# Kernel optimization log

Hardware: AMD Instinct MI355X
Metric: run time of the kernel (lower is better)

## Reference

```python
import jax, jax.numpy as jnp
import numpy as np

N_NODES = 100000
DROP_P = 0.1


def gcn_conv(x, W, b, row, col, n_nodes):
    """PyG GCNConv: out = D^{-1/2}(A+I)D^{-1/2} X W + b.
    row/col already include self-loops. Messages flow row(src) -> col(dst)."""
    xw = x @ W  # [N, H]
    deg = jax.ops.segment_sum(jnp.ones_like(col, dtype=xw.dtype), col, num_segments=n_nodes)
    dinv = jnp.where(deg > 0, jax.lax.rsqrt(deg), 0.0)
    norm = dinv[row] * dinv[col]  # [E]
    msg = norm[:, None] * xw[row]  # [E, H] gather + scale
    out = jax.ops.segment_sum(msg, col, num_segments=n_nodes)  # scatter-add
    return out + b


def dropout(x, key, p):
    keep = jax.random.bernoulli(key, 1.0 - p, x.shape)
    return jnp.where(keep, x / (1.0 - p), 0.0).astype(x.dtype)


def prelu(x, alpha):
    return jnp.where(x >= 0, x, alpha[None, :] * x)


def setup_inputs() -> dict:
    key = jax.random.key(0)
    k1, k2, k3, k4 = jax.random.split(key, 4)
    in_ch, hid = 128, 128
    n_edges = 1600000
    x = jax.random.normal(k1, (N_NODES, in_ch), dtype=jnp.float32)
    edge_index = jax.random.randint(k2, (2, n_edges), 0, N_NODES, dtype=jnp.int64)
    s = 1.0 / np.sqrt(in_ch)
    W1 = jax.random.normal(k3, (in_ch, hid), dtype=jnp.float32) * s
    W2 = jax.random.normal(k4, (hid, hid), dtype=jnp.float32) * s
    b1 = jnp.zeros((hid,), dtype=jnp.float32)
    b2 = jnp.zeros((hid,), dtype=jnp.float32)
    alpha = jnp.full((hid,), 0.25, dtype=jnp.float32)
    return {"x": x, "edge_index": edge_index, "W1": W1, "b1": b1,
            "W2": W2, "b2": b2, "alpha": alpha}


def reference(x, edge_index, W1, b1, W2, b2, alpha):
    n = x.shape[0]
    # add self-loops once (PyG default add_self_loops=True)
    loop = jnp.arange(n, dtype=edge_index.dtype)
    row = jnp.concatenate([edge_index[0], loop])
    col = jnp.concatenate([edge_index[1], loop])

    dk1, dk2 = jax.random.split(jax.random.key(42))
    h = gcn_conv(x, W1, b1, row, col, n)
    h = dropout(h, dk1, DROP_P)
    h = prelu(h, alpha)
    h = gcn_conv(h, W2, b2, row, col, n)
    h = dropout(h, dk2, DROP_P)
    h = prelu(h, alpha)
    return h
```

## Files before the change

kernel.cpp:

```cpp
#include <hip/hip_runtime.h>
#include <stdint.h>
#include <string.h>

__host__ __device__ inline uint32_t rotl32(uint32_t x, int r) {
    return (x << r) | (x >> (32 - r));
}

__host__ __device__ inline void tf2x32(uint32_t k0, uint32_t k1,
                                       uint32_t x0, uint32_t x1,
                                       uint32_t& o0, uint32_t& o1) {
    uint32_t ks0 = k0, ks1 = k1, ks2 = k0 ^ k1 ^ 0x1BD11BDAu;
    x0 += ks0; x1 += ks1;
#define TF_R4(a,b,c,d) \
    x0 += x1; x1 = rotl32(x1,a); x1 ^= x0; \
    x0 += x1; x1 = rotl32(x1,b); x1 ^= x0; \
    x0 += x1; x1 = rotl32(x1,c); x1 ^= x0; \
    x0 += x1; x1 = rotl32(x1,d); x1 ^= x0;
    TF_R4(13,15,26,6)  x0 += ks1; x1 += ks2 + 1u;
    TF_R4(17,29,16,24) x0 += ks2; x1 += ks0 + 2u;
    TF_R4(13,15,26,6)  x0 += ks0; x1 += ks1 + 3u;
    TF_R4(17,29,16,24) x0 += ks1; x1 += ks2 + 4u;
    TF_R4(13,15,26,6)  x0 += ks2; x1 += ks0 + 5u;
#undef TF_R4
    o0 = x0; o1 = x1;
}

__device__ inline unsigned pk2h(float a, float b) {
    _Float16 ha = (_Float16)a, hb = (_Float16)b;
    unsigned short ua, ub;
    __builtin_memcpy(&ua, &ha, 2);
    __builtin_memcpy(&ub, &hb, 2);
    return (unsigned)ua | ((unsigned)ub << 16);
}
__device__ inline unsigned short h16bits(float a) {
    _Float16 h = (_Float16)a;
    unsigned short u; __builtin_memcpy(&u, &h, 2);
    return u;
}
__device__ inline float lo16(unsigned u) {
    unsigned short s = (unsigned short)(u & 0xffffu);
    _Float16 h; __builtin_memcpy(&h, &s, 2);
    return (float)h;
}
__device__ inline float hi16(unsigned u) {
    unsigned short s = (unsigned short)(u >> 16);
    _Float16 h; __builtin_memcpy(&h, &s, 2);
    return (float)h;
}

typedef float fx4 __attribute__((ext_vector_type(4)));
typedef unsigned ux4 __attribute__((ext_vector_type(4)));
typedef _Float16 h16x8 __attribute__((ext_vector_type(8)));
typedef _Float16 h16x2 __attribute__((ext_vector_type(2)));
typedef float f32x4 __attribute__((ext_vector_type(4)));

__device__ inline h16x2 as_h2(unsigned u) { h16x2 r; __builtin_memcpy(&r, &u, 4); return r; }

#define CSR_CAP 48
#define NSUP 8

__global__ __launch_bounds__(256) void k_build(
        const int* __restrict__ ei, int2* __restrict__ gsup,
        unsigned* __restrict__ gsupcnt,
        unsigned long long* __restrict__ m1, unsigned long long* __restrict__ m2,
        const float* __restrict__ x, unsigned* __restrict__ xb,
        const float* __restrict__ w1, const float* __restrict__ w2,
        _Float16* __restrict__ wt1, _Float16* __restrict__ wt2,
        unsigned k1a, unsigned k1b, unsigned k2a, unsigned k2b,
        int E, int N, int supw, int scap, int total,
        int P1A, int MB, int CB) {
    int b = blockIdx.x;
    int t = (int)threadIdx.x;
    if (b < P1A) {
        __shared__ unsigned hcnt[NSUP], hoff[NSUP], hrun[NSUP];
        if (t < NSUP) { hcnt[t] = 0; hrun[t] = 0; }
        __syncthreads();
        int e0 = b * 2048 + t;
        int r[8], c[8];
        unsigned sp[8];
#pragma unroll
        for (int i = 0; i < 8; i++) {
            int e = e0 + i * 256;
            sp[i] = 0xffu;
            if (e < E) {
                c[i] = __builtin_nontemporal_load(ei + (size_t)E + e);
                r[i] = __builtin_nontemporal_load(ei + e);
                if ((unsigned)c[i] < (unsigned)N && (unsigned)r[i] < (unsigned)N) {
                    sp[i] = (unsigned)c[i] / (unsigned)supw;
                    atomicAdd(&hcnt[sp[i]], 1u);
                }
            }
        }
        __syncthreads();
        if (t < NSUP) hoff[t] = atomicAdd(&gsupcnt[t], hcnt[t]);
        __syncthreads();
#pragma unroll
        for (int i = 0; i < 8; i++) {
            if (sp[i] < (unsigned)NSUP) {
                unsigned rank = atomicAdd(&hrun[sp[i]], 1u);
                unsigned gp = hoff[sp[i]] + rank;
                if (gp < (unsigned)scap)
                    gsup[(size_t)sp[i] * scap + gp] = make_int2(r[i], c[i]);
            }
        }
        return;
    }
    b -= P1A;
    if (b < MB) {
        int wv = (b * 256 + t) >> 6;
        int lane = t & 63;
        int TW = (2 * total) >> 6;
        int half = total >> 6;
        int w0 = wv * 8;
#pragma unroll
        for (int j = 0; j < 8; j++) {
            int wd = w0 + j;
            if (wd < TW) {
                int wl = wd;
                unsigned ka = k1a, kb = k1b;
                unsigned long long* m = m1;
                if (wl >= half) { wl -= half; ka = k2a; kb = k2b; m = m2; }
                uint32_t o0, o1;
                tf2x32(ka, kb, 0u, (uint32_t)(wl * 64 + lane), o0, o1);
                bool keep = (((o0 ^ o1) >> 9) < 7549747u);
                unsigned long long bal = __ballot(keep);
                if (lane == 0)
                    __builtin_nontemporal_store(bal, m + wl);
            }
        }
        return;
    }
    b -= MB;
    if (b < CB) {
        int i = b * 256 + t;
        if (i < (total >> 3)) {
            const fx4* src = (const fx4*)(x + (size_t)i * 8);
            fx4 a = __builtin_nontemporal_load(src);
            fx4 bb = __builtin_nontemporal_load(src + 1);
            ux4 v;
            v.x = pk2h(a.x, a.y);
            v.y = pk2h(a.z, a.w);
            v.z = pk2h(bb.x, bb.y);
            v.w = pk2h(bb.z, bb.w);
            __builtin_nontemporal_store(v, (ux4*)xb + i);
        }
        return;
    }
    b -= CB;
    int idx = b * 256 + t;
    int mat = idx >> 14;
    int e2 = idx & 16383;
    int c = e2 >> 7, k = e2 & 127;
    const float* W = mat ? w2 : w1;
    _Float16* WT = mat ? wt2 : wt1;
    WT[(size_t)c * 128 + k] = (_Float16)W[(size_t)k * 128 + c];
}

__global__ __launch_bounds__(256) void k_fill2(
        const int2* __restrict__ gsup, const unsigned* __restrict__ gsupcnt,
        unsigned* __restrict__ cnt, unsigned* __restrict__ csr, int scap) {
    int s = blockIdx.x & (NSUP - 1);
    int chunk = blockIdx.x >> 3;
    unsigned ne = gsupcnt[s];
    if (ne > (unsigned)scap) ne = (unsigned)scap;
    const int2* base = gsup + (size_t)s * scap;
    unsigned e0 = (unsigned)(chunk * 2048) + threadIdx.x;
#pragma unroll
    for (int i = 0; i < 8; i++) {
        unsigned e = e0 + i * 256;
        if (e < ne) {
            int2 ed = base[e];
            unsigned c = (unsigned)ed.y;
            unsigned slot = atomicAdd(&cnt[c], 1u);
            if (slot < (unsigned)CSR_CAP)
                csr[(size_t)c * CSR_CAP + slot] = (unsigned)ed.x;
        }
    }
}

__global__ __launch_bounds__(256) void k_prep(const unsigned* __restrict__ cnt,
        float* __restrict__ dinv, uint4* __restrict__ xb4, int N) {
    int i = blockIdx.x * 256 + (int)threadIdx.x;
    int node = i >> 4, part = i & 15;
    if (node >= N) return;
    float d = rsqrtf((float)cnt[node] + 1.0f);
    if (part == 0) dinv[node] = d;
    uint4 u = xb4[(size_t)node * 16 + part];
    uint4 o;
    o.x = pk2h(d * lo16(u.x), d * hi16(u.x));
    o.y = pk2h(d * lo16(u.y), d * hi16(u.y));
    o.z = pk2h(d * lo16(u.z), d * hi16(u.z));
    o.w = pk2h(d * lo16(u.w), d * hi16(u.w));
    xb4[(size_t)node * 16 + part] = o;
}

template <int OUT_HALF>
__global__ __launch_bounds__(128, 8) void k_layer(
        const unsigned short* __restrict__ in,
        const _Float16* __restrict__ WT,
        const float* __restrict__ bias, const float* __restrict__ alpha,
        const unsigned long long* __restrict__ mask,
        const float* __restrict__ dinv, const unsigned* __restrict__ cnt,
        const unsigned* __restrict__ csr,
        void* outv, int n) {
    __shared__ unsigned hls[32 * 68];
    int t = (int)threadIdx.x;
    int wv = t >> 6;
    int l = t & 63;
    int rowbase = blockIdx.x * 32 + wv * 16;
    unsigned* hl = hls + wv * 16 * 68;
    int slot = l >> 4;
    int lm = l & 15;
    int ci = lm << 3;

    int prow = rowbase + lm;
    bool pv = prow < n;
    float dnAll = pv ? dinv[prow] : 0.f;
    unsigned cAll = pv ? cnt[prow] : 0u;
    if (cAll > (unsigned)CSR_CAP) cAll = (unsigned)CSR_CAP;

#pragma unroll
    for (int g = 0; g < 4; ++g) {
        int rloc = g * 4 + slot;
        int node = rowbase + rloc;
        float dn = __shfl(dnAll, rloc);
        unsigned ecnt = (unsigned)__shfl((int)cAll, rloc);
        h16x2 a0 = (h16x2)0, a1 = (h16x2)0, a2 = (h16x2)0, a3 = (h16x2)0;
        size_t eb = (size_t)node * CSR_CAP;
        unsigned e = 0;
        unsigned nb4 = ecnt >> 2;
#pragma unroll 2
        for (unsigned bb = 0; bb < nb4; ++bb) {
            unsigned r0 = csr[eb + e + 0];
            unsigned r1 = csr[eb + e + 1];
            unsigned r2 = csr[eb + e + 2];
            unsigned r3 = csr[eb + e + 3];
            uint4 u0 = *(const uint4*)(in + ((size_t)r0 << 7) + ci);
            uint4 u1 = *(const uint4*)(in + ((size_t)r1 << 7) + ci);
            uint4 u2 = *(const uint4*)(in + ((size_t)r2 << 7) + ci);
            uint4 u3 = *(const uint4*)(in + ((size_t)r3 << 7) + ci);
            a0 += as_h2(u0.x); a1 += as_h2(u0.y); a2 += as_h2(u0.z); a3 += as_h2(u0.w);
            a0 += as_h2(u1.x); a1 += as_h2(u1.y); a2 += as_h2(u1.z); a3 += as_h2(u1.w);
            a0 += as_h2(u2.x); a1 += as_h2(u2.y); a2 += as_h2(u2.z); a3 += as_h2(u2.w);
            a0 += as_h2(u3.x); a1 += as_h2(u3.y); a2 += as_h2(u3.z); a3 += as_h2(u3.w);
            e += 4;
        }
        for (; e < ecnt; ++e) {
            unsigned r0 = csr[eb + e];
            uint4 u0 = *(const uint4*)(in + ((size_t)r0 << 7) + ci);
            a0 += as_h2(u0.x); a1 += as_h2(u0.y); a2 += as_h2(u0.z); a3 += as_h2(u0.w);
        }
        if (node < n) {
            uint4 sv = *(const uint4*)(in + ((size_t)node << 7) + ci);
            a0 += as_h2(sv.x); a1 += as_h2(sv.y); a2 += as_h2(sv.z); a3 += as_h2(sv.w);
        }
        uint4 o;
        o.x = pk2h(dn * (float)a0[0], dn * (float)a0[1]);
        o.y = pk2h(dn * (float)a1[0], dn * (float)a1[1]);
        o.z = pk2h(dn * (float)a2[0], dn * (float)a2[1]);
        o.w = pk2h(dn * (float)a3[0], dn * (float)a3[1]);
        *(uint4*)(hl + (size_t)rloc * 68 + lm * 4) = o;
    }

    int kq = l >> 4;
    h16x8 afr[4];
#pragma unroll
    for (int kk = 0; kk < 4; kk++)
        afr[kk] = *(const h16x8*)(hl + (size_t)lm * 68 + kq * 4 + kk * 16);
#pragma unroll
    for (int f = 0; f < 8; f++) {
        f32x4 acc = (f32x4){0.f, 0.f, 0.f, 0.f};
#pragma unroll
        for (int kk = 0; kk < 4; kk++) {
            h16x8 bfr = *(const h16x8*)(WT + (size_t)(f * 16 + lm) * 128 + kk * 32 + kq * 8);
            acc = __builtin_amdgcn_mfma_f32_16x16x32_f16(afr[kk], bfr, acc, 0, 0, 0);
        }
        int c = f * 16 + lm;
        float bs = bias[c];
        float al = alpha[c];
#pragma unroll
        for (int j = 0; j < 4; j++) {
            int rl = kq * 4 + j;
            int rg = rowbase + rl;
            if (rg < n) {
                unsigned long long wmw = mask[((size_t)rg << 1) + (f >> 2)];
                bool keep = (wmw >> (c & 63)) & 1ull;
                float v = acc[j] + bs;
                v = keep ? v * (1.0f / 0.9f) : 0.0f;
                v = (v >= 0.f) ? v : al * v;
                if (OUT_HALF) {
                    float dnrow = __shfl(dnAll, rl);
                    ((unsigned short*)outv)[(size_t)rg * 128 + c] = h16bits(v * dnrow);
                } else {
                    ((float*)outv)[(size_t)rg * 128 + c] = v;
                }
            }
        }
    }
}

extern "C" void kernel_launch(void* const* d_in, const int* in_sizes, int n_in,
                              void* d_out, int out_size, void* d_ws, size_t ws_size,
                              hipStream_t stream) {
    const float* x  = (const float*)d_in[0];
    const int*   ei = (const int*)d_in[1];
    const float* W1 = (const float*)d_in[2];
    const float* b1 = (const float*)d_in[3];
    const float* W2 = (const float*)d_in[4];
    const float* b2 = (const float*)d_in[5];
    const float* al = (const float*)d_in[6];
    int N = in_sizes[0] / 128;
    int E = in_sizes[1] / 2;
    float* out = (float*)d_out;

    int supw = (N + NSUP - 1) / NSUP;
    int scap = E / NSUP + E / 64 + 4096;

    char* p = (char*)d_ws;
    unsigned short* xb = (unsigned short*)p;   p += (size_t)N * 128 * 2;
    unsigned short* ab = (unsigned short*)p;   p += (size_t)N * 128 * 2;
    int2* gsup = (int2*)ab;
    unsigned* cnt = (unsigned*)p;              p += (size_t)N * 4;
    float* dinv = (float*)p;                   p += (size_t)N * 4;
    unsigned* csr = (unsigned*)p;              p += (size_t)N * CSR_CAP * 4;
    unsigned long long* m1 = (unsigned long long*)p;  p += ((size_t)N * 128 / 64) * 8;
    unsigned long long* m2 = (unsigned long long*)p;  p += ((size_t)N * 128 / 64) * 8;
    _Float16* wt1 = (_Float16*)p;              p += 128 * 128 * 2;
    _Float16* wt2 = (_Float16*)p;              p += 128 * 128 * 2;
    unsigned* gsupcnt = (unsigned*)p;

    hipMemsetAsync(cnt, 0, (size_t)N * 4, stream);
    hipMemsetAsync(gsupcnt, 0, NSUP * 4, stream);

    uint32_t dk1a, dk1b, dk2a, dk2b;
    tf2x32(0u, 42u, 0u, 0u, dk1a, dk1b);
    tf2x32(0u, 42u, 0u, 1u, dk2a, dk2b);

    int total = N * 128;
    int P1A = (E + 2047) / 2048;
    int TW = (2 * total) / 64;
    int MB = (TW + 31) / 32;
    int CB = (total / 8 + 255) / 256;
    int WB = (2 * 128 * 128 + 255) / 256;
    k_build<<<P1A + MB + CB + WB, 256, 0, stream>>>(ei, gsup, gsupcnt, m1, m2,
                                                    x, (unsigned*)xb,
                                                    W1, W2, wt1, wt2,
                                                    dk1a, dk1b, dk2a, dk2b,
                                                    E, N, supw, scap, total,
                                                    P1A, MB, CB);
    int F2C = (scap + 2047) / 2048;
    k_fill2<<<NSUP * F2C, 256, 0, stream>>>(gsup, gsupcnt, cnt, csr, scap);
    k_prep<<<(N * 16 + 255) / 256, 256, 0, stream>>>(cnt, dinv, (uint4*)xb, N);

    int LB = (N + 31) / 32;
    k_layer<1><<<LB, 128, 0, stream>>>(xb, wt1, b1, al, m1, dinv, cnt, csr, ab, N);
    k_layer<0><<<LB, 128, 0, stream>>>(ab, wt2, b2, al, m2, dinv, cnt, csr, out, N);
}
```

Baseline: 346.8 us.

## Regroup build kernels so CSR fill overlaps mask and conversion work

Splits the edge partitioning into its own kernel and merges the CSR fill with the dropout-mask, feature-conversion and weight-transpose work in one launch, so the atomic-heavy fill runs alongside the bandwidth-bound blocks rather than serially. The layer kernel now loads four CSR indices with one vector nontemporal load, and output stores become nontemporal. This changes which work overlaps, and the vector index load assumes 16-byte alignment of each CSR row chunk, which holds given CSR_CAP=48.

```diff
diff --git a/kernel.cpp b/kernel.cpp
--- a/kernel.cpp
+++ b/kernel.cpp
@@ -59,53 +59,77 @@
 #define CSR_CAP 48
 #define NSUP 8
 
-__global__ __launch_bounds__(256) void k_build(
+__global__ __launch_bounds__(256) void k_part(
         const int* __restrict__ ei, int2* __restrict__ gsup,
-        unsigned* __restrict__ gsupcnt,
+        unsigned* __restrict__ gsupcnt, int E, int N, int supw, int scap) {
+    __shared__ unsigned hcnt[NSUP], hoff[NSUP], hrun[NSUP];
+    int b = blockIdx.x;
+    int t = (int)threadIdx.x;
+    if (t < NSUP) { hcnt[t] = 0; hrun[t] = 0; }
+    __syncthreads();
+    int e0 = b * 2048 + t;
+    int r[8], c[8];
+    unsigned sp[8];
+#pragma unroll
+    for (int i = 0; i < 8; i++) {
+        int e = e0 + i * 256;
+        sp[i] = 0xffu;
+        if (e < E) {
+            c[i] = __builtin_nontemporal_load(ei + (size_t)E + e);
+            r[i] = __builtin_nontemporal_load(ei + e);
+            if ((unsigned)c[i] < (unsigned)N && (unsigned)r[i] < (unsigned)N) {
+                sp[i] = (unsigned)c[i] / (unsigned)supw;
+                atomicAdd(&hcnt[sp[i]], 1u);
+            }
+        }
+    }
+    __syncthreads();
+    if (t < NSUP) hoff[t] = atomicAdd(&gsupcnt[t], hcnt[t]);
+    __syncthreads();
+#pragma unroll
+    for (int i = 0; i < 8; i++) {
+        if (sp[i] < (unsigned)NSUP) {
+            unsigned rank = atomicAdd(&hrun[sp[i]], 1u);
+            unsigned gp = hoff[sp[i]] + rank;
+            if (gp < (unsigned)scap)
+                gsup[(size_t)sp[i] * scap + gp] = make_int2(r[i], c[i]);
+        }
+    }
+}
+
+__global__ __launch_bounds__(256) void k_work(
+        const int2* __restrict__ gsup, const unsigned* __restrict__ gsupcnt,
+        unsigned* __restrict__ cnt, unsigned* __restrict__ csr,
         unsigned long long* __restrict__ m1, unsigned long long* __restrict__ m2,
         const float* __restrict__ x, unsigned* __restrict__ xb,
         const float* __restrict__ w1, const float* __restrict__ w2,
         _Float16* __restrict__ wt1, _Float16* __restrict__ wt2,
         unsigned k1a, unsigned k1b, unsigned k2a, unsigned k2b,
-        int E, int N, int supw, int scap, int total,
-        int P1A, int MB, int CB) {
+        int scap, int total, int FB, int MB, int CB) {
     int b = blockIdx.x;
     int t = (int)threadIdx.x;
-    if (b < P1A) {
-        __shared__ unsigned hcnt[NSUP], hoff[NSUP], hrun[NSUP];
-        if (t < NSUP) { hcnt[t] = 0; hrun[t] = 0; }
-        __syncthreads();
-        int e0 = b * 2048 + t;
-        int r[8], c[8];
-        unsigned sp[8];
+    if (b < FB) {
+        int s = b & (NSUP - 1);
+        int chunk = b >> 3;
+        unsigned ne = gsupcnt[s];
+        if (ne > (unsigned)scap) ne = (unsigned)scap;
+        const long long* base = (const long long*)(gsup + (size_t)s * scap);
+        unsigned e0 = (unsigned)(chunk * 2048) + t;
 #pragma unroll
         for (int i = 0; i < 8; i++) {
-            int e = e0 + i * 256;
-            sp[i] = 0xffu;
-            if (e < E) {
-                c[i] = __builtin_nontemporal_load(ei + (size_t)E + e);
-                r[i] = __builtin_nontemporal_load(ei + e);
-                if ((unsigned)c[i] < (unsigned)N && (unsigned)r[i] < (unsigned)N) {
-                    sp[i] = (unsigned)c[i] / (unsigned)supw;
-                    atomicAdd(&hcnt[sp[i]], 1u);
-                }
+            unsigned e = e0 + i * 256;
+            if (e < ne) {
+                long long v = __builtin_nontemporal_load(base + e);
+                unsigned r = (unsigned)(v & 0xffffffffll);
+                unsigned c = (unsigned)(v >> 32);
+                unsigned slot = atomicAdd(&cnt[c], 1u);
+                if (slot < (unsigned)CSR_CAP)
+                    csr[(size_t)c * CSR_CAP + slot] = r;
             }
         }
-        __syncthreads();
-        if (t < NSUP) hoff[t] = atomicAdd(&gsupcnt[t], hcnt[t]);
-        __syncthreads();
-#pragma unroll
-        for (int i = 0; i < 8; i++) {
-            if (sp[i] < (unsigned)NSUP) {
-                unsigned rank = atomicAdd(&hrun[sp[i]], 1u);
-                unsigned gp = hoff[sp[i]] + rank;
-                if (gp < (unsigned)scap)
-                    gsup[(size_t)sp[i] * scap + gp] = make_int2(r[i], c[i]);
-            }
-        }
         return;
     }
-    b -= P1A;
+    b -= FB;
     if (b < MB) {
         int wv = (b * 256 + t) >> 6;
         int lane = t & 63;
@@ -154,28 +178,6 @@
     const float* W = mat ? w2 : w1;
     _Float16* WT = mat ? wt2 : wt1;
     WT[(size_t)c * 128 + k] = (_Float16)W[(size_t)k * 128 + c];
-}
-
-__global__ __launch_bounds__(256) void k_fill2(
-        const int2* __restrict__ gsup, const unsigned* __restrict__ gsupcnt,
-        unsigned* __restrict__ cnt, unsigned* __restrict__ csr, int scap) {
-    int s = blockIdx.x & (NSUP - 1);
-    int chunk = blockIdx.x >> 3;
-    unsigned ne = gsupcnt[s];
-    if (ne > (unsigned)scap) ne = (unsigned)scap;
-    const int2* base = gsup + (size_t)s * scap;
-    unsigned e0 = (unsigned)(chunk * 2048) + threadIdx.x;
-#pragma unroll
-    for (int i = 0; i < 8; i++) {
-        unsigned e = e0 + i * 256;
-        if (e < ne) {
-            int2 ed = base[e];
-            unsigned c = (unsigned)ed.y;
-            unsigned slot = atomicAdd(&cnt[c], 1u);
-            if (slot < (unsigned)CSR_CAP)
-                csr[(size_t)c * CSR_CAP + slot] = (unsigned)ed.x;
-        }
-    }
 }
 
 __global__ __launch_bounds__(256) void k_prep(const unsigned* __restrict__ cnt,
@@ -231,14 +233,11 @@
         unsigned nb4 = ecnt >> 2;
 #pragma unroll 2
         for (unsigned bb = 0; bb < nb4; ++bb) {
-            unsigned r0 = csr[eb + e + 0];
-            unsigned r1 = csr[eb + e + 1];
-            unsigned r2 = csr[eb + e + 2];
-            unsigned r3 = csr[eb + e + 3];
-            uint4 u0 = *(const uint4*)(in + ((size_t)r0 << 7) + ci);
-            uint4 u1 = *(const uint4*)(in + ((size_t)r1 << 7) + ci);
-            uint4 u2 = *(const uint4*)(in + ((size_t)r2 << 7) + ci);
-            uint4 u3 = *(const uint4*)(in + ((size_t)r3 << 7) + ci);
+            ux4 rr = __builtin_nontemporal_load((const ux4*)(csr + eb + e));
+            uint4 u0 = *(const uint4*)(in + ((size_t)rr.x << 7) + ci);
+            uint4 u1 = *(const uint4*)(in + ((size_t)rr.y << 7) + ci);
+            uint4 u2 = *(const uint4*)(in + ((size_t)rr.z << 7) + ci);
+            uint4 u3 = *(const uint4*)(in + ((size_t)rr.w << 7) + ci);
             a0 += as_h2(u0.x); a1 += as_h2(u0.y); a2 += as_h2(u0.z); a3 += as_h2(u0.w);
             a0 += as_h2(u1.x); a1 += as_h2(u1.y); a2 += as_h2(u1.z); a3 += as_h2(u1.w);
             a0 += as_h2(u2.x); a1 += as_h2(u2.y); a2 += as_h2(u2.z); a3 += as_h2(u2.w);
@@ -290,9 +289,11 @@
                 v = (v >= 0.f) ? v : al * v;
                 if (OUT_HALF) {
                     float dnrow = __shfl(dnAll, rl);
-                    ((unsigned short*)outv)[(size_t)rg * 128 + c] = h16bits(v * dnrow);
+                    __builtin_nontemporal_store(h16bits(v * dnrow),
+                        (unsigned short*)outv + (size_t)rg * 128 + c);
                 } else {
-                    ((float*)outv)[(size_t)rg * 128 + c] = v;
+                    __builtin_nontemporal_store(v,
+                        (float*)outv + (size_t)rg * 128 + c);
                 }
             }
         }
@@ -338,18 +339,19 @@
 
     int total = N * 128;
     int P1A = (E + 2047) / 2048;
+    k_part<<<P1A, 256, 0, stream>>>(ei, gsup, gsupcnt, E, N, supw, scap);
+
+    int F2C = (scap + 2047) / 2048;
+    int FB = NSUP * F2C;
     int TW = (2 * total) / 64;
     int MB = (TW + 31) / 32;
     int CB = (total / 8 + 255) / 256;
     int WB = (2 * 128 * 128 + 255) / 256;
-    k_build<<<P1A + MB + CB + WB, 256, 0, stream>>>(ei, gsup, gsupcnt, m1, m2,
-                                                    x, (unsigned*)xb,
-                                                    W1, W2, wt1, wt2,
-                                                    dk1a, dk1b, dk2a, dk2b,
-                                                    E, N, supw, scap, total,
-                                                    P1A, MB, CB);
-    int F2C = (scap + 2047) / 2048;
-    k_fill2<<<NSUP * F2C, 256, 0, stream>>>(gsup, gsupcnt, cnt, csr, scap);
+    k_work<<<FB + MB + CB + WB, 256, 0, stream>>>(gsup, gsupcnt, cnt, csr,
+                                                  m1, m2, x, (unsigned*)xb,
+                                                  W1, W2, wt1, wt2,
+                                                  dk1a, dk1b, dk2a, dk2b,
+                                                  scap, total, FB, MB, CB);
     k_prep<<<(N * 16 + 255) / 256, 256, 0, stream>>>(cnt, dinv, (uint4*)xb, N);
 
     int LB = (N + 31) / 32;
```

New measurement: 347.1 us. No clear change (+0.1%).
